# Performance work log

Measured on AMD Instinct MI355X. Metric: run time of the kernel, lower is better.

The kernel has to match this reference:

```python
import jax, jax.numpy as jnp
import numpy as np

B, C, H, W = 16, 128, 128, 128


def _gram(feat):
    # feat: [B, C, H, W] -> [B, C, HW]; gram: [B, C, C]
    f = feat.reshape(feat.shape[0], feat.shape[1], -1)
    return jnp.einsum('bcn,bdn->bcd', f, f)


def setup_inputs() -> dict:
    key = jax.random.key(0)
    k1, k2 = jax.random.split(key)
    feat = jax.random.normal(k1, (B, C, H, W), dtype=jnp.float32)
    feat_decod = jax.random.normal(k2, (B, C, H, W), dtype=jnp.float32)
    return {"feat": feat, "feat_decod": feat_decod}


def reference(feat, feat_decod):
    feat_size = feat.shape[2] * feat.shape[3]  # H*W
    feat_nb = feat.shape[1]                     # C
    gram_enc = _gram(feat)
    gram_dec = _gram(feat_decod)
    diff = gram_dec - gram_enc
    # per-sample scalar loss: [B]
    denom = 4.0 * feat_size * feat_size * feat_nb * feat_nb
    return jnp.sum(diff * diff, axis=(-2, -1)) / denom
```

## Files before the change

kernel.cpp:

```cpp
#include <hip/hip_runtime.h>
#include <hip/hip_bf16.h>


typedef __attribute__((ext_vector_type(8))) short short8;
typedef __attribute__((ext_vector_type(4))) float f32x4;

#define CC 128
#define NN 16384

__device__ __forceinline__ short f2bf(float x) {
    unsigned u = __builtin_bit_cast(unsigned, x);
    u += 0x7fffu + ((u >> 16) & 1u);
    return (short)(u >> 16);
}

__global__ __launch_bounds__(256, 2) void gram_partial_k(
    const float* __restrict__ f0, const float* __restrict__ f1,
    float* __restrict__ partials, int S, int Kc, int nst)
{
    __shared__ short lds[2][CC * 64];

    const int tid = threadIdx.x;
    const int bx  = blockIdx.x;
    const int g   = bx & 31;
    const int s   = bx >> 5;

    const float* src  = (g & 1) ? f1 : f0;
    const float* base = src + (size_t)(g >> 1) * ((size_t)CC * NN) + (size_t)s * Kc;

    const int srow = tid >> 3;
    const int scb  = tid & 7;
    const float* gp = base + (size_t)srow * NN + scb * 8;

    const int lane = tid & 63;
    const int w    = tid >> 6;
    const int m0   = (w & 1) * 64;
    const int n0   = (w >> 1) * 64;
    const int lr   = lane & 15;
    const int lk   = lane >> 4;

    f32x4 acc[4][4];
    #pragma unroll
    for (int i = 0; i < 4; ++i)
        #pragma unroll
        for (int j = 0; j < 4; ++j)
            acc[i][j] = (f32x4){0.f, 0.f, 0.f, 0.f};

    float4 ra[4], rb[4];

    auto load_stage = [&](int st) {
        #pragma unroll
        for (int it = 0; it < 4; ++it) {
            const float* p = gp + (size_t)it * 32 * NN + st * 64;
            ra[it] = *(const float4*)p;
            rb[it] = *(const float4*)(p + 4);
        }
    };

    auto store_stage = [&](int buf) {
        #pragma unroll
        for (int it = 0; it < 4; ++it) {
            int r = srow + 32 * it;
            short8 v = { f2bf(ra[it].x), f2bf(ra[it].y), f2bf(ra[it].z), f2bf(ra[it].w),
                         f2bf(rb[it].x), f2bf(rb[it].y), f2bf(rb[it].z), f2bf(rb[it].w) };
            int phys = scb ^ (r & 7);
            *(short8*)&lds[buf][r * 64 + phys * 8] = v;
        }
    };

    auto compute = [&](int buf) {
        #pragma unroll
        for (int ks = 0; ks < 2; ++ks) {
            short8 af[4], bfr[4];
            int cb = ks * 4 + lk;
            #pragma unroll
            for (int i = 0; i < 4; ++i) {
                int r = m0 + i * 16 + lr;
                af[i] = *(const short8*)&lds[buf][r * 64 + ((cb ^ (r & 7)) * 8)];
            }
            #pragma unroll
            for (int i = 0; i < 4; ++i) {
                int r = n0 + i * 16 + lr;
                bfr[i] = *(const short8*)&lds[buf][r * 64 + ((cb ^ (r & 7)) * 8)];
            }
            #pragma unroll
            for (int mi = 0; mi < 4; ++mi)
                #pragma unroll
                for (int ni = 0; ni < 4; ++ni)
                    acc[mi][ni] = __builtin_amdgcn_mfma_f32_16x16x32_bf16(
                        af[mi], bfr[ni], acc[mi][ni], 0, 0, 0);
        }
    };

    load_stage(0);
    store_stage(0);
    __syncthreads();
    for (int st = 0; st < nst; ++st) {
        int cur = st & 1;
        bool more = (st + 1 < nst);
        if (more) load_stage(st + 1);
        compute(cur);
        if (more) store_stage(cur ^ 1);
        __syncthreads();
    }

    float* op = partials + ((size_t)g * S + s) * (CC * CC);
    #pragma unroll
    for (int mi = 0; mi < 4; ++mi)
        #pragma unroll
        for (int ni = 0; ni < 4; ++ni)
            #pragma unroll
            for (int i = 0; i < 4; ++i) {
                int row = m0 + mi * 16 + lk * 4 + i;
                int col = n0 + ni * 16 + lr;
                op[row * CC + col] = acc[mi][ni][i];
            }
}

__global__ __launch_bounds__(256) void reduce1_k(
    const float* __restrict__ partials, float* __restrict__ part2, int S)
{
    int b     = blockIdx.x >> 6;
    int chunk = blockIdx.x & 63;
    int t     = threadIdx.x;
    int e     = chunk * 256 + t;

    const float* Pe = partials + ((size_t)(2 * b) * S) * (CC * CC) + e;
    const float* Pd = partials + ((size_t)(2 * b + 1) * S) * (CC * CC) + e;
    float ae = 0.f, ad = 0.f;
    for (int s = 0; s < S; ++s) {
        ae += Pe[(size_t)s * (CC * CC)];
        ad += Pd[(size_t)s * (CC * CC)];
    }
    float d = ad - ae;
    float v = d * d;
    #pragma unroll
    for (int off = 32; off > 0; off >>= 1) v += __shfl_down(v, off);
    __shared__ float wsum[4];
    if ((t & 63) == 0) wsum[t >> 6] = v;
    __syncthreads();
    if (t == 0) part2[b * 64 + chunk] = wsum[0] + wsum[1] + wsum[2] + wsum[3];
}

__global__ void reduce2_k(const float* __restrict__ part2, float* __restrict__ out)
{
    int b = blockIdx.x;
    int t = threadIdx.x;
    float v = part2[b * 64 + t];
    #pragma unroll
    for (int off = 32; off > 0; off >>= 1) v += __shfl_down(v, off);
    if (t == 0) out[b] = v * (1.0f / 17592186044416.0f);
}

extern "C" void kernel_launch(void* const* d_in, const int* in_sizes, int n_in,
                              void* d_out, int out_size, void* d_ws, size_t ws_size,
                              hipStream_t stream)
{
    const float* f0 = (const float*)d_in[0];
    const float* f1 = (const float*)d_in[1];
    float* out = (float*)d_out;

    const size_t perS = 32ull * CC * CC * 4;
    const size_t tail = 16 * 64 * 4;
    int S = 16;
    while (S > 1 && perS * (size_t)S + tail > ws_size) S >>= 1;
    int Kc  = NN / S;
    int nst = Kc / 64;

    float* partials = (float*)d_ws;
    float* part2    = (float*)((char*)d_ws + perS * (size_t)S);

    gram_partial_k<<<32 * S, 256, 0, stream>>>(f0, f1, partials, S, Kc, nst);
    reduce1_k<<<16 * 64, 256, 0, stream>>>(partials, part2, S);
    reduce2_k<<<16, 64, 0, stream>>>(part2, out);
}
```

Measured before the change: 291.7 us.

## Double K-tile depth, rotate stage start per block, vectorize partial reduction

Doubles the K depth of each staged tile from 64 to 128 columns. Each stage now issues 8 row loads per thread and runs 4 MFMA k-steps between barriers, which halves the number of sync/stage iterations. Each block's starting stage is rotated by its block index to spread concurrent DRAM accesses. The reduce kernel now reads float4 vectors, uses 16 chunks per sample instead of 64, and fully unrolls the S=16 case. In exchange, LDS grows to 64KB per block and the register count rises, which may limit the two-blocks-per-CU occupancy.

```diff
diff --git a/kernel.cpp b/kernel.cpp
--- a/kernel.cpp
+++ b/kernel.cpp
@@ -18,7 +18,7 @@
     const float* __restrict__ f0, const float* __restrict__ f1,
     float* __restrict__ partials, int S, int Kc, int nst)
 {
-    __shared__ short lds[2][CC * 64];
+    __shared__ short lds[2][CC * 128];
 
     const int tid = threadIdx.x;
     const int bx  = blockIdx.x;
@@ -28,8 +28,8 @@
     const float* src  = (g & 1) ? f1 : f0;
     const float* base = src + (size_t)(g >> 1) * ((size_t)CC * NN) + (size_t)s * Kc;
 
-    const int srow = tid >> 3;
-    const int scb  = tid & 7;
+    const int srow = tid >> 4;
+    const int scb  = tid & 15;
     const float* gp = base + (size_t)srow * NN + scb * 8;
 
     const int lane = tid & 63;
@@ -39,6 +39,8 @@
     const int lr   = lane & 15;
     const int lk   = lane >> 4;
 
+    const int rot = bx & (nst - 1);
+
     f32x4 acc[4][4];
     #pragma unroll
     for (int i = 0; i < 4; ++i)
@@ -46,12 +48,13 @@
         for (int j = 0; j < 4; ++j)
             acc[i][j] = (f32x4){0.f, 0.f, 0.f, 0.f};
 
-    float4 ra[4], rb[4];
+    float4 ra[8], rb[8];
 
     auto load_stage = [&](int st) {
+        int sp = (st + rot) & (nst - 1);
         #pragma unroll
-        for (int it = 0; it < 4; ++it) {
-            const float* p = gp + (size_t)it * 32 * NN + st * 64;
+        for (int it = 0; it < 8; ++it) {
+            const float* p = gp + (size_t)it * 16 * NN + (size_t)sp * 128;
             ra[it] = *(const float4*)p;
             rb[it] = *(const float4*)(p + 4);
         }
@@ -59,29 +62,29 @@
 
     auto store_stage = [&](int buf) {
         #pragma unroll
-        for (int it = 0; it < 4; ++it) {
-            int r = srow + 32 * it;
+        for (int it = 0; it < 8; ++it) {
+            int r = srow + 16 * it;
             short8 v = { f2bf(ra[it].x), f2bf(ra[it].y), f2bf(ra[it].z), f2bf(ra[it].w),
                          f2bf(rb[it].x), f2bf(rb[it].y), f2bf(rb[it].z), f2bf(rb[it].w) };
-            int phys = scb ^ (r & 7);
-            *(short8*)&lds[buf][r * 64 + phys * 8] = v;
+            int phys = scb ^ (r & 15);
+            *(short8*)&lds[buf][r * 128 + phys * 8] = v;
         }
     };
 
     auto compute = [&](int buf) {
         #pragma unroll
-        for (int ks = 0; ks < 2; ++ks) {
+        for (int ks = 0; ks < 4; ++ks) {
             short8 af[4], bfr[4];
             int cb = ks * 4 + lk;
             #pragma unroll
             for (int i = 0; i < 4; ++i) {
                 int r = m0 + i * 16 + lr;
-                af[i] = *(const short8*)&lds[buf][r * 64 + ((cb ^ (r & 7)) * 8)];
+                af[i] = *(const short8*)&lds[buf][r * 128 + ((cb ^ (r & 15)) * 8)];
             }
             #pragma unroll
             for (int i = 0; i < 4; ++i) {
                 int r = n0 + i * 16 + lr;
-                bfr[i] = *(const short8*)&lds[buf][r * 64 + ((cb ^ (r & 7)) * 8)];
+                bfr[i] = *(const short8*)&lds[buf][r * 128 + ((cb ^ (r & 15)) * 8)];
             }
             #pragma unroll
             for (int mi = 0; mi < 4; ++mi)
@@ -120,35 +123,45 @@
 __global__ __launch_bounds__(256) void reduce1_k(
     const float* __restrict__ partials, float* __restrict__ part2, int S)
 {
-    int b     = blockIdx.x >> 6;
-    int chunk = blockIdx.x & 63;
+    int b     = blockIdx.x >> 4;
+    int chunk = blockIdx.x & 15;
     int t     = threadIdx.x;
-    int e     = chunk * 256 + t;
+    size_t e  = (size_t)chunk * 1024 + (size_t)t * 4;
 
-    const float* Pe = partials + ((size_t)(2 * b) * S) * (CC * CC) + e;
-    const float* Pd = partials + ((size_t)(2 * b + 1) * S) * (CC * CC) + e;
-    float ae = 0.f, ad = 0.f;
-    for (int s = 0; s < S; ++s) {
-        ae += Pe[(size_t)s * (CC * CC)];
-        ad += Pd[(size_t)s * (CC * CC)];
+    const f32x4* Pe = (const f32x4*)(partials + ((size_t)(2 * b) * S) * (CC * CC) + e);
+    const f32x4* Pd = (const f32x4*)(partials + ((size_t)(2 * b + 1) * S) * (CC * CC) + e);
+    const size_t stride = (size_t)CC * CC / 4;
+
+    f32x4 ae = {0.f, 0.f, 0.f, 0.f}, ad = {0.f, 0.f, 0.f, 0.f};
+    if (S == 16) {
+        #pragma unroll
+        for (int s2 = 0; s2 < 16; ++s2) {
+            ae += Pe[(size_t)s2 * stride];
+            ad += Pd[(size_t)s2 * stride];
+        }
+    } else {
+        for (int s2 = 0; s2 < S; ++s2) {
+            ae += Pe[(size_t)s2 * stride];
+            ad += Pd[(size_t)s2 * stride];
+        }
     }
-    float d = ad - ae;
-    float v = d * d;
+    f32x4 d = ad - ae;
+    float v = d[0] * d[0] + d[1] * d[1] + d[2] * d[2] + d[3] * d[3];
     #pragma unroll
     for (int off = 32; off > 0; off >>= 1) v += __shfl_down(v, off);
     __shared__ float wsum[4];
     if ((t & 63) == 0) wsum[t >> 6] = v;
     __syncthreads();
-    if (t == 0) part2[b * 64 + chunk] = wsum[0] + wsum[1] + wsum[2] + wsum[3];
+    if (t == 0) part2[b * 16 + chunk] = wsum[0] + wsum[1] + wsum[2] + wsum[3];
 }
 
 __global__ void reduce2_k(const float* __restrict__ part2, float* __restrict__ out)
 {
     int b = blockIdx.x;
     int t = threadIdx.x;
-    float v = part2[b * 64 + t];
+    float v = (t < 16) ? part2[b * 16 + t] : 0.f;
     #pragma unroll
-    for (int off = 32; off > 0; off >>= 1) v += __shfl_down(v, off);
+    for (int off = 8; off > 0; off >>= 1) v += __shfl_down(v, off);
     if (t == 0) out[b] = v * (1.0f / 17592186044416.0f);
 }
 
@@ -161,16 +174,16 @@
     float* out = (float*)d_out;
 
     const size_t perS = 32ull * CC * CC * 4;
-    const size_t tail = 16 * 64 * 4;
+    const size_t tail = 16 * 16 * 4;
     int S = 16;
     while (S > 1 && perS * (size_t)S + tail > ws_size) S >>= 1;
     int Kc  = NN / S;
-    int nst = Kc / 64;
+    int nst = Kc / 128;
 
     float* partials = (float*)d_ws;
     float* part2    = (float*)((char*)d_ws + perS * (size_t)S);
 
     gram_partial_k<<<32 * S, 256, 0, stream>>>(f0, f1, partials, S, Kc, nst);
-    reduce1_k<<<16 * 64, 256, 0, stream>>>(partials, part2, S);
+    reduce1_k<<<16 * 16, 256, 0, stream>>>(partials, part2, S);
     reduce2_k<<<16, 64, 0, stream>>>(part2, out);
 }
```

Measured after the change: 289.7 us. No clear change (-0.7%).
